# Performance work log

Measured on AMD Instinct MI355X. Metric: run time of the kernel, lower is better.

Reference implementation:

```python
import jax, jax.numpy as jnp
import numpy as np

B, N, M, D, V = 16, 2048, 2048, 128, 128


def setup_inputs() -> dict:
    key0 = jax.random.key(0)
    kq, kk, kv, kp = jax.random.split(key0, 4)
    return {
        "query": jax.random.normal(kq, (B, N, D), dtype=jnp.float32),
        "key": jax.random.normal(kk, (B, M, D), dtype=jnp.float32),
        "value": jax.random.normal(kv, (B, M, V), dtype=jnp.float32),
        "key_padding_len": jax.random.randint(kp, (B,), 0, 512),
        "is_attn_mask_len": 1,  # Python int -> causal masking on
    }


def reference(query, key, value, key_padding_len, is_attn_mask_len):
    # query:[B,N,D], key:[B,M,D], value:[B,M,V], key_padding_len:[B]
    Bq, Nq, Dq = query.shape
    Mk = key.shape[1]
    scale = 1.0 / jnp.sqrt(jnp.asarray(Dq, dtype=query.dtype))

    # torch mask(): zero out the LAST key_padding_len key positions
    pos = jnp.arange(Mk)
    keep = pos[None, :] < (Mk - key_padding_len)[:, None]  # [B,M]
    key = jnp.where(keep[:, :, None], key, jnp.zeros((), key.dtype))

    score = jnp.einsum("bnd,bmd->bnm", query, key) * scale  # [B,N,M]

    if is_attn_mask_len:
        # attn_mask_len[b,i] = M-1-i  ->  row i keeps positions j <= i (causal)
        causal = pos[None, :] <= jnp.arange(Nq)[:, None]  # [N,M]
        score = jnp.where(causal[None, :, :], score, jnp.asarray(-1e6, score.dtype))

    attn = jax.nn.softmax(score, axis=-1)  # dropout p=0 -> identity
    out = jnp.einsum("bnm,bmv->bnv", attn, value)  # [B,N,V]
    return out
```

## Files before the change

### kernel.cpp

```cpp
#include <hip/hip_runtime.h>
#include <stdint.h>

typedef unsigned short ushort_t;
typedef __attribute__((ext_vector_type(8))) short short8;
typedef __attribute__((ext_vector_type(4))) float floatx4;

#define SEQ_N 2048
#define SEQ_M 2048
#define DIM_D 128
#define DIM_V 128
#define BC 64

#define KS_LD 136
#define VS_LD 72
#define PS_LD 72
#define KB(i) ((i) * 8704)
#define VB(i) (17408 + (i) * 9216)
#define P0 35840
#define SMEM_ELEMS 40448

#define WS_O_FLOATS (256 * 2 * 64 * 128)
#define WS_M_OFF    WS_O_FLOATS
#define WS_L_OFF    (WS_O_FLOATS + 32768)
#define WS_FLOATS   (WS_O_FLOATS + 65536)

#if __has_builtin(__builtin_amdgcn_exp2f)
#define EXP2F(x) __builtin_amdgcn_exp2f(x)
#else
#define EXP2F(x) exp2f(x)
#endif

template <int CTRL>
__device__ __forceinline__ float dpp_f(float x) {
  int xi = __builtin_bit_cast(int, x);
  int yi = __builtin_amdgcn_update_dpp(xi, xi, CTRL, 0xf, 0xf, false);
  return __builtin_bit_cast(float, yi);
}
__device__ __forceinline__ float rowmax16(float x) {
  x = fmaxf(x, dpp_f<0x128>(x));
  x = fmaxf(x, dpp_f<0x124>(x));
  x = fmaxf(x, dpp_f<0x122>(x));
  x = fmaxf(x, dpp_f<0x121>(x));
  return x;
}
__device__ __forceinline__ float rowsum16(float x) {
  x += dpp_f<0x128>(x);
  x += dpp_f<0x124>(x);
  x += dpp_f<0x122>(x);
  x += dpp_f<0x121>(x);
  return x;
}

__device__ __forceinline__ ushort_t f2bf(float f) {
  uint32_t u = __builtin_bit_cast(uint32_t, f);
  return (ushort_t)((u + 0x8000u) >> 16);
}
__device__ __forceinline__ uint32_t bfpack(float lo, float hi) {
  uint32_t a = __builtin_bit_cast(uint32_t, lo) + 0x8000u;
  uint32_t b = __builtin_bit_cast(uint32_t, hi) + 0x8000u;
  return __builtin_amdgcn_perm(b, a, 0x07060302u);
}

__device__ __forceinline__ void process_chunk(
    const float* __restrict__ Q, const float* __restrict__ K,
    const float* __restrict__ Vg, float* __restrict__ Out,
    float* __restrict__ ws, ushort_t* __restrict__ smem,
    int b, int rt, int jt_lo, int jt_hi, int mlimit, int flag, int c, bool direct) {
  const int tid  = threadIdx.x;
  const int lane = tid & 63;
  const int w    = tid >> 6;
  const int qd   = lane >> 4;
  const int nn   = lane & 15;

  const float c1 = 0.08838834764831845f * 1.4426950408889634f;

  const int oct = tid & 15;
  const int j0  = (tid >> 4) * 4;
  const int hh  = nn >> 3;
  const int rb  = 8 * hh;

  const int i0w = rt * 64 + w * 16;
  const size_t koff = (size_t)b * SEQ_M * DIM_D;
  const size_t voff = (size_t)b * SEQ_M * DIM_V;

  short8 qf[4];
  {
    const float* Qb = Q + ((size_t)b * SEQ_N + (size_t)(i0w + nn)) * DIM_D;
    union { short8 v; uint32_t u32[4]; } t;
#pragma unroll
    for (int ks = 0; ks < 4; ++ks) {
      const float* p = Qb + ks * 32 + qd * 8;
      float4 f0 = *(const float4*)p, f1 = *(const float4*)(p + 4);
      t.u32[0] = bfpack(f0.x, f0.y);
      t.u32[1] = bfpack(f0.z, f0.w);
      t.u32[2] = bfpack(f1.x, f1.y);
      t.u32[3] = bfpack(f1.z, f1.w);
      qf[ks] = t.v;
    }
  }

  floatx4 o[8];
#pragma unroll
  for (int vt = 0; vt < 8; ++vt) o[vt] = (floatx4)0.0f;
  float m[4], l[4];
#pragma unroll
  for (int r = 0; r < 4; ++r) { m[r] = -3.0e38f; l[r] = 0.0f; }

  float4 kr[4][2], vr[4][2];

  auto stage_load = [&](int jt) {
    const int jbase = jt * BC;
#pragma unroll
    for (int r = 0; r < 4; ++r) {
      const float* kp = K  + koff + (size_t)(jbase + j0 + r) * DIM_D + oct * 8;
      kr[r][0] = *(const float4*)kp;  kr[r][1] = *(const float4*)(kp + 4);
      const float* vp = Vg + voff + (size_t)(jbase + j0 + r) * DIM_V + oct * 8;
      vr[r][0] = *(const float4*)vp;  vr[r][1] = *(const float4*)(vp + 4);
    }
  };

  auto stage_write = [&](int buf, int jt) {
    const int jbase = jt * BC;
    const int kb = KB(buf), vb = VB(buf);
#pragma unroll
    for (int r = 0; r < 4; ++r) {
      uint4 kw;
      kw.x = bfpack(kr[r][0].x, kr[r][0].y);
      kw.y = bfpack(kr[r][0].z, kr[r][0].w);
      kw.z = bfpack(kr[r][1].x, kr[r][1].y);
      kw.w = bfpack(kr[r][1].z, kr[r][1].w);
      if (jbase + j0 + r >= mlimit) kw = make_uint4(0u, 0u, 0u, 0u);
      *(uint4*)(smem + kb + (j0 + r) * KS_LD + oct * 8) = kw;
    }
    float vc[4][8];
#pragma unroll
    for (int r = 0; r < 4; ++r) {
      vc[r][0]=vr[r][0].x; vc[r][1]=vr[r][0].y; vc[r][2]=vr[r][0].z; vc[r][3]=vr[r][0].w;
      vc[r][4]=vr[r][1].x; vc[r][5]=vr[r][1].y; vc[r][6]=vr[r][1].z; vc[r][7]=vr[r][1].w;
    }
#pragma unroll
    for (int q = 0; q < 8; ++q) {
      const int p = 8 * oct + ((oct + q) & 7);
      uint2 dv;
      dv.x = bfpack(vc[0][q], vc[1][q]);
      dv.y = bfpack(vc[2][q], vc[3][q]);
      *(uint2*)(smem + vb + p * VS_LD + j0) = dv;
    }
  };

  stage_load(jt_lo);
  stage_write(0, jt_lo);
  __syncthreads();

  const int len = jt_hi - jt_lo;
#pragma unroll 1
  for (int t = 0; t < len; ++t) {
    const int jt = jt_lo + t;
    const int cur = t & 1;
    const bool more = (t + 1) < len;
    const int jbase = jt * BC;
    if (more) stage_load(jt + 1);

    const int kb = KB(cur), vb = VB(cur);

    floatx4 s[4];
#pragma unroll
    for (int ct = 0; ct < 4; ++ct) s[ct] = (floatx4)0.0f;
#pragma unroll
    for (int ks = 0; ks < 4; ++ks) {
#pragma unroll
      for (int ct = 0; ct < 4; ++ct) {
        short8 bf = *(const short8*)(smem + kb + (ct * 16 + nn) * KS_LD + ks * 32 + qd * 8);
        s[ct] = __builtin_amdgcn_mfma_f32_16x16x32_bf16(qf[ks], bf, s[ct], 0, 0, 0);
      }
    }

    {
      float tt[4][4];
      const bool needmask = flag && (jbase + BC - 1 > i0w);
#pragma unroll
      for (int ct = 0; ct < 4; ++ct)
#pragma unroll
        for (int r = 0; r < 4; ++r) {
          float tv = s[ct][r] * c1;
          if (needmask) {
            int jgl = jbase + ct * 16 + nn;
            int igl = i0w + qd * 4 + r;
            if (jgl > igl) tv = -3.0e38f;
          }
          tt[ct][r] = tv;
        }
#pragma unroll
      for (int r = 0; r < 4; ++r) {
        float mr = fmaxf(fmaxf(tt[0][r], tt[1][r]), fmaxf(tt[2][r], tt[3][r]));
        mr = rowmax16(mr);
        float mn = fmaxf(m[r], mr);
        float alpha = EXP2F(m[r] - mn);
        m[r] = mn;
        float ps = 0.0f;
#pragma unroll
        for (int ct = 0; ct < 4; ++ct) {
          float p = EXP2F(tt[ct][r] - mn);
          tt[ct][r] = p;
          ps += p;
        }
        l[r] = l[r] * alpha + ps;
#pragma unroll
        for (int vt = 0; vt < 8; ++vt) o[vt][r] *= alpha;
      }
#pragma unroll
      for (int ct = 0; ct < 4; ++ct)
#pragma unroll
        for (int r = 0; r < 4; ++r)
          smem[P0 + (w * 16 + qd * 4 + r) * PS_LD + ct * 16 + nn] = f2bf(tt[ct][r]);
    }

#pragma unroll
    for (int ks2 = 0; ks2 < 2; ++ks2) {
      short8 a = *(const short8*)(smem + P0 + (w * 16 + nn) * PS_LD + ks2 * 32 + qd * 8);
#pragma unroll
      for (int vt = 0; vt < 8; ++vt) {
        const int p = 16 * vt + rb + ((2 * vt + nn + hh) & 7);
        short8 vbf = *(const short8*)(smem + vb + p * VS_LD + ks2 * 32 + qd * 8);
        o[vt] = __builtin_amdgcn_mfma_f32_16x16x32_bf16(a, vbf, o[vt], 0, 0, 0);
      }
    }

    if (more) stage_write(cur ^ 1, jt + 1);
    __syncthreads();
  }

#pragma unroll
  for (int r = 0; r < 4; ++r) l[r] = rowsum16(l[r]);

  if (direct) {
    float* Ob = Out + ((size_t)b * SEQ_N + i0w) * DIM_V;
#pragma unroll
    for (int r = 0; r < 4; ++r) {
      float inv = 1.0f / l[r];
      int row = qd * 4 + r;
#pragma unroll
      for (int vt = 0; vt < 8; ++vt)
        Ob[(size_t)row * DIM_V + vt * 16 + nn] = o[vt][r] * inv;
    }
  } else {
    const int p = b * 16 + (rt - 16);
    const int slot = p * 2 + c;
    float* Op = ws + (size_t)slot * 64 * 128;
#pragma unroll
    for (int r = 0; r < 4; ++r) {
      int row = w * 16 + qd * 4 + r;
#pragma unroll
      for (int vt = 0; vt < 8; ++vt)
        Op[(size_t)row * 128 + vt * 16 + nn] = o[vt][r];
    }
    if (nn == 0) {
#pragma unroll
      for (int r = 0; r < 4; ++r) {
        int row = w * 16 + qd * 4 + r;
        ws[WS_M_OFF + slot * 64 + row] = m[r];
        ws[WS_L_OFF + slot * 64 + row] = l[r];
      }
    }
  }
}

__global__ __launch_bounds__(256, 2)
void fa_chunk(const float* __restrict__ Q, const float* __restrict__ K,
              const float* __restrict__ Vg, const int* __restrict__ kpl,
              const int* __restrict__ amask, float* __restrict__ Out,
              float* __restrict__ ws) {
  __shared__ __align__(16) ushort_t smem[SMEM_ELEMS];
  const int bx = blockIdx.x;
  const int b  = bx & 15;
  const int u  = bx >> 4;
  int rt, c;
  if (u < 16)      { rt = 16 + u; c = 0; }
  else if (u < 32) { rt = 47 - u; c = 1; }
  else             { rt = 47 - u; c = 0; }
  const int flag   = amask[0];
  const int mlimit = SEQ_M - kpl[b];
  const int ntiles = flag ? (rt + 1) : (SEQ_M / BC);
  const int jt_lo  = (c == 1) ? 16 : 0;
  const int jt_hi  = (c == 0 && rt >= 16) ? 16 : ntiles;
  process_chunk(Q, K, Vg, Out, ws, smem, b, rt, jt_lo, jt_hi, mlimit, flag, c, rt < 16);
}

__global__ __launch_bounds__(256)
void fa_merge(const float* __restrict__ ws, float* __restrict__ Out) {
  const int w = threadIdx.x >> 6, lane = threadIdx.x & 63;
  const int rowid = blockIdx.x * 4 + w;
  const int p = rowid >> 6, rr = rowid & 63;
  const int b = p >> 4, rt = 16 + (p & 15);
  float m1 = ws[WS_M_OFF + (p * 2 + 0) * 64 + rr];
  float l1 = ws[WS_L_OFF + (p * 2 + 0) * 64 + rr];
  float m2 = ws[WS_M_OFF + (p * 2 + 1) * 64 + rr];
  float l2 = ws[WS_L_OFF + (p * 2 + 1) * 64 + rr];
  float M  = fmaxf(m1, m2);
  float a1 = EXP2F(m1 - M), a2 = EXP2F(m2 - M);
  float inv = 1.0f / (l1 * a1 + l2 * a2);
  const float* O1 = ws + ((size_t)(p * 2 + 0) * 64 + rr) * 128;
  const float* O2 = ws + ((size_t)(p * 2 + 1) * 64 + rr) * 128;
  float2 x1 = *(const float2*)(O1 + lane * 2);
  float2 x2 = *(const float2*)(O2 + lane * 2);
  float2 r;
  r.x = (x1.x * a1 + x2.x * a2) * inv;
  r.y = (x1.y * a1 + x2.y * a2) * inv;
  *(float2*)(Out + ((size_t)b * SEQ_N + rt * 64 + rr) * 128 + lane * 2) = r;
}

__global__ __launch_bounds__(256, 2)
void fa_paired(const float* __restrict__ Q, const float* __restrict__ K,
               const float* __restrict__ Vg, const int* __restrict__ kpl,
               const int* __restrict__ amask, float* __restrict__ Out) {
  __shared__ __align__(16) ushort_t smem[SMEM_ELEMS];
  const int bx = blockIdx.x;
  const int b  = bx & 15;
  const int pp = bx >> 4;
  const int flag   = amask[0];
  const int mlimit = SEQ_M - kpl[b];
#pragma unroll 1
  for (int ph = 0; ph < 2; ++ph) {
    const int rt = ph ? (31 - pp) : pp;
    const int ntiles = flag ? (rt + 1) : (SEQ_M / BC);
    process_chunk(Q, K, Vg, Out, nullptr, smem, b, rt, 0, ntiles, mlimit, flag, 0, true);
  }
}

extern "C" void kernel_launch(void* const* d_in, const int* in_sizes, int n_in,
                              void* d_out, int out_size, void* d_ws, size_t ws_size,
                              hipStream_t stream) {
  const float* Q   = (const float*)d_in[0];
  const float* K   = (const float*)d_in[1];
  const float* V   = (const float*)d_in[2];
  const int* kpl   = (const int*)d_in[3];
  const int* amask = (const int*)d_in[4];
  float* O         = (float*)d_out;
  float* ws        = (float*)d_ws;

  if (ws_size >= (size_t)WS_FLOATS * 4) {
    hipLaunchKernelGGL(fa_chunk, dim3(768), dim3(256), 0, stream, Q, K, V, kpl, amask, O, ws);
    hipLaunchKernelGGL(fa_merge, dim3(4096), dim3(256), 0, stream, ws, O);
  } else {
    hipLaunchKernelGGL(fa_paired, dim3(256), dim3(256), 0, stream, Q, K, V, kpl, amask, O);
  }
}
```

Before: 145.5 us.

## Split long causal row tiles into up to four KV chunks with bf16 partial merge

Replaces the two-way split-K scheme with a variable split (1 to 4 chunks per row tile, by causal length), giving 1280 blocks of more even work. Shared memory drops to a single K/V buffer so three blocks fit per CU, at the cost of an extra barrier per tile and losing the load/compute overlap. Partial outputs are stored normalized in bf16, and the first chunk writes straight to the output, which the merge kernel rescales in place. The softmax scale is folded into Q, and the rescale of O is skipped when no row max changes across the wave.

```diff
diff --git a/kernel.cpp b/kernel.cpp
--- a/kernel.cpp
+++ b/kernel.cpp
@@ -13,16 +13,14 @@
 
 #define KS_LD 136
 #define VS_LD 72
-#define PS_LD 72
-#define KB(i) ((i) * 8704)
-#define VB(i) (17408 + (i) * 9216)
-#define P0 35840
-#define SMEM_ELEMS 40448
-
-#define WS_O_FLOATS (256 * 2 * 64 * 128)
-#define WS_M_OFF    WS_O_FLOATS
-#define WS_L_OFF    (WS_O_FLOATS + 32768)
-#define WS_FLOATS   (WS_O_FLOATS + 65536)
+#define PS_LD 68
+#define K0 0
+#define V0 8704
+#define P0 17920
+#define SMEM_ELEMS 22272
+
+#define ML_FLOATS (16 * 72 * 2 * 64)
+#define WS_BYTES  ((size_t)ML_FLOATS * 4 + (size_t)16 * 48 * 64 * 128 * 2)
 
 #if __has_builtin(__builtin_amdgcn_exp2f)
 #define EXP2F(x) __builtin_amdgcn_exp2f(x)
@@ -60,12 +58,16 @@
   uint32_t b = __builtin_bit_cast(uint32_t, hi) + 0x8000u;
   return __builtin_amdgcn_perm(b, a, 0x07060302u);
 }
+__device__ __forceinline__ float bf2f(uint32_t u16) {
+  return __builtin_bit_cast(float, u16 << 16);
+}
 
 __device__ __forceinline__ void process_chunk(
     const float* __restrict__ Q, const float* __restrict__ K,
     const float* __restrict__ Vg, float* __restrict__ Out,
     float* __restrict__ ws, ushort_t* __restrict__ smem,
-    int b, int rt, int jt_lo, int jt_hi, int mlimit, int flag, int c, bool direct) {
+    int b, int rt, int jt_lo, int jt_hi, int mlimit, int flag,
+    int nch, int slot, int oidx) {
   const int tid  = threadIdx.x;
   const int lane = tid & 63;
   const int w    = tid >> 6;
@@ -91,10 +93,10 @@
     for (int ks = 0; ks < 4; ++ks) {
       const float* p = Qb + ks * 32 + qd * 8;
       float4 f0 = *(const float4*)p, f1 = *(const float4*)(p + 4);
-      t.u32[0] = bfpack(f0.x, f0.y);
-      t.u32[1] = bfpack(f0.z, f0.w);
-      t.u32[2] = bfpack(f1.x, f1.y);
-      t.u32[3] = bfpack(f1.z, f1.w);
+      t.u32[0] = bfpack(f0.x * c1, f0.y * c1);
+      t.u32[1] = bfpack(f0.z * c1, f0.w * c1);
+      t.u32[2] = bfpack(f1.x * c1, f1.y * c1);
+      t.u32[3] = bfpack(f1.z * c1, f1.w * c1);
       qf[ks] = t.v;
     }
   }
@@ -119,9 +121,8 @@
     }
   };
 
-  auto stage_write = [&](int buf, int jt) {
+  auto stage_write = [&](int jt) {
     const int jbase = jt * BC;
-    const int kb = KB(buf), vb = VB(buf);
 #pragma unroll
     for (int r = 0; r < 4; ++r) {
       uint4 kw;
@@ -130,7 +131,7 @@
       kw.z = bfpack(kr[r][1].x, kr[r][1].y);
       kw.w = bfpack(kr[r][1].z, kr[r][1].w);
       if (jbase + j0 + r >= mlimit) kw = make_uint4(0u, 0u, 0u, 0u);
-      *(uint4*)(smem + kb + (j0 + r) * KS_LD + oct * 8) = kw;
+      *(uint4*)(smem + K0 + (j0 + r) * KS_LD + oct * 8) = kw;
     }
     float vc[4][8];
 #pragma unroll
@@ -144,25 +145,22 @@
       uint2 dv;
       dv.x = bfpack(vc[0][q], vc[1][q]);
       dv.y = bfpack(vc[2][q], vc[3][q]);
-      *(uint2*)(smem + vb + p * VS_LD + j0) = dv;
+      *(uint2*)(smem + V0 + p * VS_LD + j0) = dv;
     }
   };
 
   stage_load(jt_lo);
-  stage_write(0, jt_lo);
+  stage_write(jt_lo);
   __syncthreads();
 
   const int len = jt_hi - jt_lo;
 #pragma unroll 1
   for (int t = 0; t < len; ++t) {
     const int jt = jt_lo + t;
-    const int cur = t & 1;
     const bool more = (t + 1) < len;
     const int jbase = jt * BC;
     if (more) stage_load(jt + 1);
 
-    const int kb = KB(cur), vb = VB(cur);
-
     floatx4 s[4];
 #pragma unroll
     for (int ct = 0; ct < 4; ++ct) s[ct] = (floatx4)0.0f;
@@ -170,43 +168,56 @@
     for (int ks = 0; ks < 4; ++ks) {
 #pragma unroll
       for (int ct = 0; ct < 4; ++ct) {
-        short8 bf = *(const short8*)(smem + kb + (ct * 16 + nn) * KS_LD + ks * 32 + qd * 8);
+        short8 bf = *(const short8*)(smem + K0 + (ct * 16 + nn) * KS_LD + ks * 32 + qd * 8);
         s[ct] = __builtin_amdgcn_mfma_f32_16x16x32_bf16(qf[ks], bf, s[ct], 0, 0, 0);
       }
     }
 
     {
       float tt[4][4];
-      const bool needmask = flag && (jbase + BC - 1 > i0w);
-#pragma unroll
-      for (int ct = 0; ct < 4; ++ct)
-#pragma unroll
-        for (int r = 0; r < 4; ++r) {
-          float tv = s[ct][r] * c1;
-          if (needmask) {
-            int jgl = jbase + ct * 16 + nn;
-            int igl = i0w + qd * 4 + r;
-            if (jgl > igl) tv = -3.0e38f;
+      if (flag && (jbase + BC - 1 > i0w)) {
+#pragma unroll
+        for (int ct = 0; ct < 4; ++ct)
+#pragma unroll
+          for (int r = 0; r < 4; ++r) {
+            float tv = s[ct][r];
+            if (jbase + ct * 16 + nn > i0w + qd * 4 + r) tv = -3.0e38f;
+            tt[ct][r] = tv;
           }
-          tt[ct][r] = tv;
-        }
+      } else {
+#pragma unroll
+        for (int ct = 0; ct < 4; ++ct)
+#pragma unroll
+          for (int r = 0; r < 4; ++r) tt[ct][r] = s[ct][r];
+      }
+      float mn[4];
 #pragma unroll
       for (int r = 0; r < 4; ++r) {
         float mr = fmaxf(fmaxf(tt[0][r], tt[1][r]), fmaxf(tt[2][r], tt[3][r]));
         mr = rowmax16(mr);
-        float mn = fmaxf(m[r], mr);
-        float alpha = EXP2F(m[r] - mn);
-        m[r] = mn;
+        mn[r] = fmaxf(m[r], mr);
+      }
+      int same = (mn[0] == m[0]) && (mn[1] == m[1]) && (mn[2] == m[2]) && (mn[3] == m[3]);
+      if (!__all(same)) {
+#pragma unroll
+        for (int r = 0; r < 4; ++r) {
+          float alpha = EXP2F(m[r] - mn[r]);
+          l[r] *= alpha;
+#pragma unroll
+          for (int vt = 0; vt < 8; ++vt) o[vt][r] *= alpha;
+        }
+      }
+#pragma unroll
+      for (int r = 0; r < 4; ++r) {
+        m[r] = mn[r];
         float ps = 0.0f;
 #pragma unroll
         for (int ct = 0; ct < 4; ++ct) {
-          float p = EXP2F(tt[ct][r] - mn);
+          float p = EXP2F(tt[ct][r] - m[r]);
           tt[ct][r] = p;
           ps += p;
         }
-        l[r] = l[r] * alpha + ps;
-#pragma unroll
-        for (int vt = 0; vt < 8; ++vt) o[vt][r] *= alpha;
+        l[r] += ps;
       }
 #pragma unroll
       for (int ct = 0; ct < 4; ++ct)
@@ -221,19 +232,30 @@
 #pragma unroll
       for (int vt = 0; vt < 8; ++vt) {
         const int p = 16 * vt + rb + ((2 * vt + nn + hh) & 7);
-        short8 vbf = *(const short8*)(smem + vb + p * VS_LD + ks2 * 32 + qd * 8);
+        short8 vbf = *(const short8*)(smem + V0 + p * VS_LD + ks2 * 32 + qd * 8);
         o[vt] = __builtin_amdgcn_mfma_f32_16x16x32_bf16(a, vbf, o[vt], 0, 0, 0);
       }
     }
 
-    if (more) stage_write(cur ^ 1, jt + 1);
     __syncthreads();
+    if (more) { stage_write(jt + 1); __syncthreads(); }
   }
 
 #pragma unroll
   for (int r = 0; r < 4; ++r) l[r] = rowsum16(l[r]);
 
-  if (direct) {
+  if (nch > 1) {
+    float* mlp = ws + (size_t)(b * 72 + slot) * 2 * 64;
+    if (nn == 0) {
+#pragma unroll
+      for (int r = 0; r < 4; ++r) {
+        int row = w * 16 + qd * 4 + r;
+        mlp[row]      = m[r];
+        mlp[64 + row] = l[r];
+      }
+    }
+  }
+  if (nch == 1 || oidx < 0) {
     float* Ob = Out + ((size_t)b * SEQ_N + i0w) * DIM_V;
 #pragma unroll
     for (int r = 0; r < 4; ++r) {
@@ -244,87 +266,111 @@
         Ob[(size_t)row * DIM_V + vt * 16 + nn] = o[vt][r] * inv;
     }
   } else {
-    const int p = b * 16 + (rt - 16);
-    const int slot = p * 2 + c;
-    float* Op = ws + (size_t)slot * 64 * 128;
-#pragma unroll
-    for (int r = 0; r < 4; ++r) {
+    ushort_t* ob = (ushort_t*)(ws + ML_FLOATS) + (size_t)(b * 48 + oidx) * 64 * 128;
+#pragma unroll
+    for (int r = 0; r < 4; ++r) {
+      float inv = 1.0f / l[r];
       int row = w * 16 + qd * 4 + r;
 #pragma unroll
       for (int vt = 0; vt < 8; ++vt)
-        Op[(size_t)row * 128 + vt * 16 + nn] = o[vt][r];
-    }
-    if (nn == 0) {
-#pragma unroll
-      for (int r = 0; r < 4; ++r) {
-        int row = w * 16 + qd * 4 + r;
-        ws[WS_M_OFF + slot * 64 + row] = m[r];
-        ws[WS_L_OFF + slot * 64 + row] = l[r];
-      }
-    }
-  }
-}
-
-__global__ __launch_bounds__(256, 2)
+        ob[row * 128 + vt * 16 + nn] = f2bf(o[vt][r] * inv);
+    }
+  }
+}
+
+__global__ __launch_bounds__(256, 3)
 void fa_chunk(const float* __restrict__ Q, const float* __restrict__ K,
               const float* __restrict__ Vg, const int* __restrict__ kpl,
               const int* __restrict__ amask, float* __restrict__ Out,
-              float* __restrict__ ws) {
+              float* __restrict__ ws, int mode) {
   __shared__ __align__(16) ushort_t smem[SMEM_ELEMS];
-  const int bx = blockIdx.x;
-  const int b  = bx & 15;
-  const int u  = bx >> 4;
-  int rt, c;
-  if (u < 16)      { rt = 16 + u; c = 0; }
-  else if (u < 32) { rt = 47 - u; c = 1; }
-  else             { rt = 47 - u; c = 0; }
-  const int flag   = amask[0];
+  const int u = blockIdx.x;
+  const int b = u & 15;
+  const int idx = u >> 4;
+  const int flag = amask[0];
   const int mlimit = SEQ_M - kpl[b];
-  const int ntiles = flag ? (rt + 1) : (SEQ_M / BC);
-  const int jt_lo  = (c == 1) ? 16 : 0;
-  const int jt_hi  = (c == 0 && rt >= 16) ? 16 : ntiles;
-  process_chunk(Q, K, Vg, Out, ws, smem, b, rt, jt_lo, jt_hi, mlimit, flag, c, rt < 16);
+
+  if (mode == 0) {
+    int rt = 31 - idx;
+    int hi = flag ? (rt + 1) : (SEQ_M / BC);
+    process_chunk(Q, K, Vg, Out, ws, smem, b, rt, 0, hi, mlimit, flag, 1, 0, -1);
+    return;
+  }
+  if (flag) {
+    int rt, c, nch;
+    if (idx < 32)      { rt = 31 - (idx >> 2); c = idx & 3; nch = 4; }
+    else if (idx < 56) { int t = idx - 32; int q3 = t / 3; rt = 23 - q3; c = t - 3 * q3; nch = 3; }
+    else if (idx < 72) { int t = idx - 56; rt = 15 - (t >> 1); c = t & 1; nch = 2; }
+    else               { rt = 79 - idx; c = 0; nch = 1; }
+    const int tiles = rt + 1;
+    const int lo = (c * tiles) / nch, hi = ((c + 1) * tiles) / nch;
+    int slot = 0, oidx = -1;
+    if (nch > 1) {
+      int sb = (rt >= 24) ? 40 + (rt - 24) * 4 : (rt >= 16) ? 16 + (rt - 16) * 3 : (rt - 8) * 2;
+      slot = sb + c;
+      if (c > 0)
+        oidx = (rt >= 24) ? 24 + (rt - 24) * 3 + (c - 1)
+             : (rt >= 16) ? 8 + (rt - 16) * 2 + (c - 1)
+                          : (rt - 8) + (c - 1);
+    }
+    process_chunk(Q, K, Vg, Out, ws, smem, b, rt, lo, hi, mlimit, flag, nch, slot, oidx);
+  } else {
+    if (u >= 1024) return;
+    const int rt = 31 - (idx >> 1), c = idx & 1;
+    process_chunk(Q, K, Vg, Out, ws, smem, b, rt, c * 16, c * 16 + 16, mlimit, 0,
+                  2, rt * 2 + c, (c > 0) ? rt : -1);
+  }
 }
 
 __global__ __launch_bounds__(256)
-void fa_merge(const float* __restrict__ ws, float* __restrict__ Out) {
+void fa_merge(float* __restrict__ ws, float* __restrict__ Out,
+              const int* __restrict__ amask) {
+  const int flag = amask[0];
   const int w = threadIdx.x >> 6, lane = threadIdx.x & 63;
-  const int rowid = blockIdx.x * 4 + w;
-  const int p = rowid >> 6, rr = rowid & 63;
-  const int b = p >> 4, rt = 16 + (p & 15);
-  float m1 = ws[WS_M_OFF + (p * 2 + 0) * 64 + rr];
-  float l1 = ws[WS_L_OFF + (p * 2 + 0) * 64 + rr];
-  float m2 = ws[WS_M_OFF + (p * 2 + 1) * 64 + rr];
-  float l2 = ws[WS_L_OFF + (p * 2 + 1) * 64 + rr];
-  float M  = fmaxf(m1, m2);
-  float a1 = EXP2F(m1 - M), a2 = EXP2F(m2 - M);
-  float inv = 1.0f / (l1 * a1 + l2 * a2);
-  const float* O1 = ws + ((size_t)(p * 2 + 0) * 64 + rr) * 128;
-  const float* O2 = ws + ((size_t)(p * 2 + 1) * 64 + rr) * 128;
-  float2 x1 = *(const float2*)(O1 + lane * 2);
-  float2 x2 = *(const float2*)(O2 + lane * 2);
-  float2 r;
-  r.x = (x1.x * a1 + x2.x * a2) * inv;
-  r.y = (x1.y * a1 + x2.y * a2) * inv;
-  *(float2*)(Out + ((size_t)b * SEQ_N + rt * 64 + rr) * 128 + lane * 2) = r;
-}
-
-__global__ __launch_bounds__(256, 2)
-void fa_paired(const float* __restrict__ Q, const float* __restrict__ K,
-               const float* __restrict__ Vg, const int* __restrict__ kpl,
-               const int* __restrict__ amask, float* __restrict__ Out) {
-  __shared__ __align__(16) ushort_t smem[SMEM_ELEMS];
-  const int bx = blockIdx.x;
-  const int b  = bx & 15;
-  const int pp = bx >> 4;
-  const int flag   = amask[0];
-  const int mlimit = SEQ_M - kpl[b];
-#pragma unroll 1
-  for (int ph = 0; ph < 2; ++ph) {
-    const int rt = ph ? (31 - pp) : pp;
-    const int ntiles = flag ? (rt + 1) : (SEQ_M / BC);
-    process_chunk(Q, K, Vg, Out, nullptr, smem, b, rt, 0, ntiles, mlimit, flag, 0, true);
-  }
+  const int rid = blockIdx.x * 4 + w;
+  int b, rt, row, nch, sb, ob;
+  if (flag) {
+    if (rid >= 24576) return;
+    b = rid / 1536; int rr = rid - b * 1536;
+    rt = 8 + (rr >> 6); row = rr & 63;
+    nch = (rt >= 24) ? 4 : (rt >= 16) ? 3 : 2;
+    sb  = (rt >= 24) ? 40 + (rt - 24) * 4 : (rt >= 16) ? 16 + (rt - 16) * 3 : (rt - 8) * 2;
+    ob  = (rt >= 24) ? 24 + (rt - 24) * 3 : (rt >= 16) ? 8 + (rt - 16) * 2 : (rt - 8);
+  } else {
+    if (rid >= 32768) return;
+    b = rid >> 11; int rr = rid & 2047;
+    rt = rr >> 6; row = rr & 63;
+    nch = 2; sb = rt * 2; ob = rt;
+  }
+  float mm[4], ll[4];
+  float M = -3.0e38f;
+#pragma unroll
+  for (int cc = 0; cc < 4; ++cc) if (cc < nch) {
+    const float* mlp = ws + (size_t)(b * 72 + sb + cc) * 2 * 64;
+    mm[cc] = mlp[row];
+    ll[cc] = mlp[64 + row];
+    M = fmaxf(M, mm[cc]);
+  }
+  float wc[4], wsum = 0.0f;
+#pragma unroll
+  for (int cc = 0; cc < 4; ++cc) if (cc < nch) {
+    wc[cc] = ll[cc] * EXP2F(mm[cc] - M);
+    wsum += wc[cc];
+  }
+  const float inv = 1.0f / wsum;
+  float* orow = Out + ((size_t)b * SEQ_N + rt * 64 + row) * DIM_V;
+  float2 acc = *(float2*)(orow + lane * 2);
+  acc.x *= wc[0]; acc.y *= wc[0];
+  const ushort_t* Obf = (const ushort_t*)(ws + ML_FLOATS);
+#pragma unroll
+  for (int cc = 1; cc < 4; ++cc) if (cc < nch) {
+    const ushort_t* pr = Obf + ((size_t)(b * 48 + ob + cc - 1) * 64 + row) * 128;
+    uint32_t v = *(const uint32_t*)(pr + lane * 2);
+    acc.x += bf2f(v & 0xffffu) * wc[cc];
+    acc.y += bf2f(v >> 16)     * wc[cc];
+  }
+  acc.x *= inv; acc.y *= inv;
+  *(float2*)(orow + lane * 2) = acc;
 }
 
 extern "C" void kernel_launch(void* const* d_in, const int* in_sizes, int n_in,
@@ -338,10 +384,10 @@
   float* O         = (float*)d_out;
   float* ws        = (float*)d_ws;
 
-  if (ws_size >= (size_t)WS_FLOATS * 4) {
-    hipLaunchKernelGGL(fa_chunk, dim3(768), dim3(256), 0, stream, Q, K, V, kpl, amask, O, ws);
-    hipLaunchKernelGGL(fa_merge, dim3(4096), dim3(256), 0, stream, ws, O);
+  if (ws_size >= WS_BYTES) {
+    hipLaunchKernelGGL(fa_chunk, dim3(1280), dim3(256), 0, stream, Q, K, V, kpl, amask, O, ws, 1);
+    hipLaunchKernelGGL(fa_merge, dim3(8192), dim3(256), 0, stream, ws, O, amask);
   } else {
-    hipLaunchKernelGGL(fa_paired, dim3(256), dim3(256), 0, stream, Q, K, V, kpl, amask, O);
-  }
-}
+    hipLaunchKernelGGL(fa_chunk, dim3(512), dim3(256), 0, stream, Q, K, V, kpl, amask, O, ws, 0);
+  }
+}
```

Measured after the change: 185.2 us. 27.2% more time.
